# Kernel tuning notes

Hardware: AMD Instinct MI355X
Metric: run time of the kernel (lower is better)

## Reference

```python
import jax, jax.numpy as jnp
import numpy as np

H, CM, CS = 8, 16, 32  # num_heads, hidden_mv_channels, hidden_s_channels
_INNER_IDX = np.array([0, 2, 3, 4, 8, 9, 10, 14])  # PGA multivector components without e0


def _make_basis():
    # 9 Pin(3,0,1)-equivariant linear maps on 16-dim multivectors:
    # 5 grade projections + 4 left-multiplications by e0 (grade k -> grade k+1 e0-blades).
    # Component order: [1, e0, e1, e2, e3, e01, e02, e03, e12, e13, e23, e012, e013, e023, e123, e0123]
    b = np.zeros((9, 16, 16), dtype=np.float32)
    grades = [[0], [1, 2, 3, 4], [5, 6, 7, 8, 9, 10], [11, 12, 13, 14], [15]]
    for k, idxs in enumerate(grades):
        for i in idxs:
            b[k, i, i] = 1.0
    e0maps = {5: [(0, 1)], 6: [(2, 5), (3, 6), (4, 7)], 7: [(8, 11), (9, 12), (10, 13)], 8: [(14, 15)]}
    for k, pairs in e0maps.items():
        for i, o in pairs:
            b[k, o, i] = 1.0
    return jnp.asarray(b)


BASIS = _make_basis()  # (9, 16_out_comp, 16_in_comp)


def equi_linear(mv, s, w_mv, w_s2mv, b_mv, w_mv2s, w_s2s, b_s):
    # mv: (..., c_in, 16); s: (..., s_in)
    out_mv = jnp.einsum('yai,ocy,...ci->...oa', BASIS, w_mv, mv)
    out_mv = out_mv.at[..., 0].add(jnp.einsum('...i,oi->...o', s, w_s2mv) + b_mv)
    out_s = (jnp.einsum('...c,sc->...s', mv[..., 0], w_mv2s)
             + jnp.einsum('...i,si->...s', s, w_s2s) + b_s)
    return out_mv, out_s


def reference(multivectors_kv, multivectors_q, scalars_kv, scalars_q,
              q_w_mv, q_w_s2mv, q_b_mv, q_w_mv2s, q_w_s2s, q_b_s,
              k_w_mv, k_w_s2mv, k_b_mv, k_w_mv2s, k_w_s2s, k_b_s,
              v_w_mv, v_w_s2mv, v_b_mv, v_w_mv2s, v_w_s2s, v_b_s,
              o_w_mv, o_w_s2mv, o_b_mv, o_w_mv2s, o_w_s2s, o_b_s):
    B, Q = multivectors_q.shape[0], multivectors_q.shape[1]
    q_mv, q_s = equi_linear(multivectors_q, scalars_q, q_w_mv, q_w_s2mv, q_b_mv, q_w_mv2s, q_w_s2s, q_b_s)
    k_mv, k_s = equi_linear(multivectors_kv, scalars_kv, k_w_mv, k_w_s2mv, k_b_mv, k_w_mv2s, k_w_s2s, k_b_s)
    v_mv, v_s = equi_linear(multivectors_kv, scalars_kv, v_w_mv, v_w_s2mv, v_b_mv, v_w_mv2s, v_w_s2s, v_b_s)
    # split heads; einops pattern '(hidden_channels num_heads)' => channel-major, head-minor
    q_mv = q_mv.reshape(B, Q, CM, H, 16).transpose(0, 3, 1, 2, 4)  # (B,H,Q,CM,16)
    q_s = q_s.reshape(B, Q, CS, H).transpose(0, 3, 1, 2)            # (B,H,Q,CS)
    # multi-query: single k/v head broadcast over H
    scale = 1.0 / jnp.sqrt(jnp.asarray(8 * CM + CS, dtype=q_mv.dtype))
    scores = (jnp.einsum('bhqcx,bkcx->bhqk', q_mv[..., _INNER_IDX], k_mv[..., _INNER_IDX])
              + jnp.einsum('bhqs,bks->bhqk', q_s, k_s)) * scale
    attn = jax.nn.softmax(scores, axis=-1)
    h_mv = jnp.einsum('bhqk,bkcx->bhqcx', attn, v_mv)
    h_s = jnp.einsum('bhqk,bkc->bhqc', attn, v_s)
    # merge heads; pattern '(n_heads hidden_channels)' => head-major
    h_mv = h_mv.transpose(0, 2, 1, 3, 4).reshape(B, Q, H * CM, 16)
    h_s = h_s.transpose(0, 2, 1, 3).reshape(B, Q, H * CS)
    out_mv, out_s = equi_linear(h_mv, h_s, o_w_mv, o_w_s2mv, o_b_mv, o_w_mv2s, o_w_s2s, o_b_s)
    return out_mv, out_s


def setup_inputs():
    key = jax.random.key(0)
    ks = jax.random.split(key, 32)
    B, NQ, NKV, IN_MV, IN_S = 4, 2048, 2048, 16, 32
    w = 0.05  # weight scale to keep attention logits sane

    def rn(k, shape, s=1.0):
        return jax.random.normal(k, shape, dtype=jnp.float32) * s

    return {
        'multivectors_kv': rn(ks[0], (B, NKV, IN_MV, 16)),
        'multivectors_q': rn(ks[1], (B, NQ, IN_MV, 16)),
        'scalars_kv': rn(ks[2], (B, NKV, IN_S)),
        'scalars_q': rn(ks[3], (B, NQ, IN_S)),
        'q_w_mv': rn(ks[4], (CM * H, IN_MV, 9), w),
        'q_w_s2mv': rn(ks[5], (CM * H, IN_S), w),
        'q_b_mv': jnp.zeros((CM * H,), jnp.float32),
        'q_w_mv2s': rn(ks[6], (CS * H, IN_MV), w),
        'q_w_s2s': rn(ks[7], (CS * H, IN_S), w),
        'q_b_s': jnp.zeros((CS * H,), jnp.float32),
        'k_w_mv': rn(ks[8], (CM, IN_MV, 9), w),
        'k_w_s2mv': rn(ks[9], (CM, IN_S), w),
        'k_b_mv': jnp.zeros((CM,), jnp.float32),
        'k_w_mv2s': rn(ks[10], (CS, IN_MV), w),
        'k_w_s2s': rn(ks[11], (CS, IN_S), w),
        'k_b_s': jnp.zeros((CS,), jnp.float32),
        'v_w_mv': rn(ks[12], (CM, IN_MV, 9), w),
        'v_w_s2mv': rn(ks[13], (CM, IN_S), w),
        'v_b_mv': jnp.zeros((CM,), jnp.float32),
        'v_w_mv2s': rn(ks[14], (CS, IN_MV), w),
        'v_w_s2s': rn(ks[15], (CS, IN_S), w),
        'v_b_s': jnp.zeros((CS,), jnp.float32),
        'o_w_mv': rn(ks[16], (16, CM * H, 9), w),
        'o_w_s2mv': rn(ks[17], (16, CS * H), w),
        'o_b_mv': jnp.zeros((16,), jnp.float32),
        'o_w_mv2s': rn(ks[18], (32, CM * H), w),
        'o_w_s2s': rn(ks[19], (32, CS * H), w),
        'o_b_s': jnp.zeros((32,), jnp.float32),
    }
```

## Files before the change

kernel.cpp:

```cpp
#include <hip/hip_runtime.h>
#include <hip/hip_bf16.h>
#include <math.h>

#define NB   4
#define NQL  2048
#define NKVL 2048
#define HN   8
#define DQK  160
#define DV   288
#define QT   256
#define KTL  64
#define KLP  168

#define SCALE 0.07905694150420949f

typedef __attribute__((ext_vector_type(8)))  short short8;
typedef __attribute__((ext_vector_type(4)))  float f32x4;
typedef __attribute__((ext_vector_type(16))) float f32x16;

__constant__ int c_grade[16] = {0,1,1,1,1,2,2,2,2,2,2,3,3,3,3,4};
__constant__ int c_inner[8]  = {0,2,3,4,8,9,10,14};
__constant__ int c_esrc[16]  = {-1,0,-1,-1,-1,2,3,4,-1,-1,-1,8,9,10,-1,14};
__constant__ int c_ey[16]    = {0,5,0,0,0,6,6,6,0,0,0,7,7,7,0,8};

__device__ __forceinline__ ushort f2bf(float v) {
  __hip_bfloat16 h = __float2bfloat16(v);
  union { __hip_bfloat16 b; ushort u; } cv; cv.b = h; return cv.u;
}

__device__ __forceinline__ void gload16(const void* g, void* l) {
  __builtin_amdgcn_global_load_lds(
      (const __attribute__((address_space(1))) unsigned int*)g,
      (__attribute__((address_space(3))) unsigned int*)l, 16, 0, 0);
}

#define KWMV   0
#define KS2MV  2304
#define KMV2S  2816
#define KS2S   3328
#define KBMV   4352
#define KBS    4368
#define VWMV   4400
#define VS2MV  6704
#define VMV2S  7216
#define VS2S   7728
#define VBMV   8752
#define VBS    8768
#define WLSZ   8800
#define XSTR   289
#define OSTR   456
#define KVPOS  8

__device__ __forceinline__ void kv_accum(const float* wL, const float* xL,
                                         int f, float acc[KVPOS]) {
  if (f < 160) {
    if (f < 128) {
      int c = f >> 3, a = c_inner[f & 7], y = c_grade[a];
      float bias = (a == 0) ? wL[KBMV + c] : 0.f;
#pragma unroll
      for (int p = 0; p < KVPOS; p++) acc[p] = bias;
      for (int ci = 0; ci < 16; ci++) {
        float w = wL[KWMV + (c*16 + ci)*9 + y];
#pragma unroll
        for (int p = 0; p < KVPOS; p++) acc[p] += w * xL[p*XSTR + ci*16 + a];
      }
      if (a == 0) {
        for (int i2 = 0; i2 < 32; i2++) {
          float w = wL[KS2MV + c*32 + i2];
#pragma unroll
          for (int p = 0; p < KVPOS; p++) acc[p] += w * xL[p*XSTR + 256 + i2];
        }
      }
    } else {
      int si = f - 128;
      float bias = wL[KBS + si];
#pragma unroll
      for (int p = 0; p < KVPOS; p++) acc[p] = bias;
      for (int ci = 0; ci < 16; ci++) {
        float w = wL[KMV2S + si*16 + ci];
#pragma unroll
        for (int p = 0; p < KVPOS; p++) acc[p] += w * xL[p*XSTR + ci*16];
      }
      for (int i2 = 0; i2 < 32; i2++) {
        float w = wL[KS2S + si*32 + i2];
#pragma unroll
        for (int p = 0; p < KVPOS; p++) acc[p] += w * xL[p*XSTR + 256 + i2];
      }
    }
  } else {
    int g = f - 160;
    if (g < 256) {
      int c = g >> 4, a = g & 15, y = c_grade[a];
      float bias = (a == 0) ? wL[VBMV + c] : 0.f;
#pragma unroll
      for (int p = 0; p < KVPOS; p++) acc[p] = bias;
      for (int ci = 0; ci < 16; ci++) {
        float w = wL[VWMV + (c*16 + ci)*9 + y];
#pragma unroll
        for (int p = 0; p < KVPOS; p++) acc[p] += w * xL[p*XSTR + ci*16 + a];
      }
      int sa = c_esrc[a];
      if (sa >= 0) {
        int ey = c_ey[a];
        for (int ci = 0; ci < 16; ci++) {
          float w = wL[VWMV + (c*16 + ci)*9 + ey];
#pragma unroll
          for (int p = 0; p < KVPOS; p++) acc[p] += w * xL[p*XSTR + ci*16 + sa];
        }
      }
      if (a == 0) {
        for (int i2 = 0; i2 < 32; i2++) {
          float w = wL[VS2MV + c*32 + i2];
#pragma unroll
          for (int p = 0; p < KVPOS; p++) acc[p] += w * xL[p*XSTR + 256 + i2];
        }
      }
    } else {
      int si = g - 256;
      float bias = wL[VBS + si];
#pragma unroll
      for (int p = 0; p < KVPOS; p++) acc[p] = bias;
      for (int ci = 0; ci < 16; ci++) {
        float w = wL[VMV2S + si*16 + ci];
#pragma unroll
        for (int p = 0; p < KVPOS; p++) acc[p] += w * xL[p*XSTR + ci*16];
      }
      for (int i2 = 0; i2 < 32; i2++) {
        float w = wL[VS2S + si*32 + i2];
#pragma unroll
        for (int p = 0; p < KVPOS; p++) acc[p] += w * xL[p*XSTR + 256 + i2];
      }
    }
  }
}

__global__ __launch_bounds__(256) void proj_kv_kernel(
    const float* __restrict__ mv_kv, const float* __restrict__ s_kv,
    const float* __restrict__ kw_mv, const float* __restrict__ kw_s2mv, const float* __restrict__ kb_mv,
    const float* __restrict__ kw_mv2s, const float* __restrict__ kw_s2s, const float* __restrict__ kb_s,
    const float* __restrict__ vw_mv, const float* __restrict__ vw_s2mv, const float* __restrict__ vb_mv,
    const float* __restrict__ vw_mv2s, const float* __restrict__ vw_s2s, const float* __restrict__ vb_s,
    ushort* __restrict__ Kf, ushort* __restrict__ VfT)
{
  __shared__ float wL[WLSZ];
  __shared__ float xL[KVPOS*XSTR];
  int t = threadIdx.x;
  for (int i = t; i < 2304; i += 256) wL[KWMV + i] = kw_mv[i];
  for (int i = t; i < 512;  i += 256) wL[KS2MV + i] = kw_s2mv[i];
  for (int i = t; i < 512;  i += 256) wL[KMV2S + i] = kw_mv2s[i];
  for (int i = t; i < 1024; i += 256) wL[KS2S + i] = kw_s2s[i];
  if (t < 16) wL[KBMV + t] = kb_mv[t];
  if (t < 32) wL[KBS + t] = kb_s[t];
  for (int i = t; i < 2304; i += 256) wL[VWMV + i] = vw_mv[i];
  for (int i = t; i < 512;  i += 256) wL[VS2MV + i] = vw_s2mv[i];
  for (int i = t; i < 512;  i += 256) wL[VMV2S + i] = vw_mv2s[i];
  for (int i = t; i < 1024; i += 256) wL[VS2S + i] = vw_s2s[i];
  if (t < 16) wL[VBMV + t] = vb_mv[t];
  if (t < 32) wL[VBS + t] = vb_s[t];

  int p0 = blockIdx.x * KVPOS;
  for (int i = t; i < KVPOS*256; i += 256) {
    int p = i >> 8, c = i & 255;
    xL[p*XSTR + c] = mv_kv[(size_t)(p0 + p)*256 + c];
  }
  if (t < KVPOS*32) {
    int p = t >> 5, c = t & 31;
    xL[p*XSTR + 256 + c] = s_kv[(size_t)(p0 + p)*32 + c];
  }
  __syncthreads();

  float acc0[KVPOS], acc1[KVPOS];
  kv_accum(wL, xL, t, acc0);
  if (t < 192) kv_accum(wL, xL, 256 + t, acc1);
  __syncthreads();

  ushort* oL = (ushort*)xL;
#pragma unroll
  for (int p = 0; p < KVPOS; p++) oL[p*OSTR + t] = f2bf(acc0[p]);
  if (t < 192) {
#pragma unroll
    for (int p = 0; p < KVPOS; p++) oL[p*OSTR + 256 + t] = f2bf(acc1[p]);
  }
  __syncthreads();

  int b = p0 >> 11, kv0 = p0 & 2047;
  for (int it = 0; it < 3; it++) {
    int j = t + it*256;
    if (j < KVPOS*80) {
      int p = j / 80, fp = j - p*80;
      uint u = (uint)oL[p*OSTR + 2*fp] | ((uint)oL[p*OSTR + 2*fp + 1] << 16);
      *(uint*)(Kf + (size_t)(p0 + p)*DQK + 2*fp) = u;
    }
  }
  for (int it = 0; it < 5; it++) {
    int j = t + it*256;
    if (j < DV*(KVPOS/2)) {
      int g = j >> 2, pp = j & 3;
      uint u = (uint)oL[(2*pp)*OSTR + 160 + g] | ((uint)oL[(2*pp+1)*OSTR + 160 + g] << 16);
      int kv = kv0 + 2*pp;
      int pos = (kv & ~63) + ((((kv >> 3) & 7) ^ (g & 7)) << 3) + (kv & 7);
      *(uint*)(VfT + ((size_t)b*DV + g)*NKVL + pos) = u;
    }
  }
}

#define OWT_SZ 34816
#define QWT_MV 0
#define QWT_S  20480
#define QBT    61440
#define QWT_SZ 62720
__global__ __launch_bounds__(256) void prep_w_kernel(
    const float* __restrict__ ow_mv, const float* __restrict__ ow_s2mv,
    const float* __restrict__ ow_mv2s, const float* __restrict__ ow_s2s,
    float* __restrict__ owT,
    const float* __restrict__ qw_mv, const float* __restrict__ qw_s2mv, const float* __restrict__ qb_mv,
    const float* __restrict__ qw_mv2s, const float* __restrict__ qw_s2s, const float* __restrict__ qb_s,
    float* __restrict__ qwT)
{
  int i = blockIdx.x*256 + threadIdx.x;
  if (i < OWT_SZ) {
    if (i < 18432) {
      int y = i / 2048, r = i & 2047, ch = r >> 4, o = r & 15;
      owT[i] = ow_mv[(size_t)(o*128 + ch)*9 + y];
    } else if (i < 22528) {
      int r = i - 18432, jj = r >> 4, o = r & 15;
      owT[i] = ow_s2mv[o*256 + jj];
    } else if (i < 26624) {
      int r = i - 22528, ch = r >> 5, si = r & 31;
      owT[i] = ow_mv2s[si*128 + ch];
    } else {
      int r = i - 26624, jj = r >> 5, si = r & 31;
      owT[i] = ow_s2s[si*256 + jj];
    }
    return;
  }
  int j = i - OWT_SZ;
  if (j >= QWT_SZ) return;
  if (j < QWT_S) {
    int ci = j / 1280, r = j - ci*1280, h = r / 160, f0 = r - h*160;
    float v;
    if (f0 < 128) {
      int c = f0 >> 3, a = c_inner[f0 & 7], y = c_grade[a];
      v = qw_mv[((c*HN + h)*16 + ci)*9 + y];
    } else {
      v = qw_mv2s[((f0 - 128)*HN + h)*16 + ci];
    }
    qwT[j] = v;
  } else if (j < QBT) {
    int k = j - QWT_S;
    int i2 = k / 1280, r = k - i2*1280, h = r / 160, f0 = r - h*160;
    float v;
    if (f0 < 128) {
      int c = f0 >> 3, a = c_inner[f0 & 7];
      v = (a == 0) ? qw_s2mv[(c*HN + h)*32 + i2] : 0.f;
    } else {
      v = qw_s2s[((f0 - 128)*HN + h)*32 + i2];
    }
    qwT[j] = v;
  } else {
    int r = j - QBT, h = r / 160, f0 = r - h*160;
    float v;
    if (f0 < 128) {
      int c = f0 >> 3, a = c_inner[f0 & 7];
      v = (a == 0) ? qb_mv[c*HN + h] : 0.f;
    } else {
      v = qb_s[(f0 - 128)*HN + h];
    }
    qwT[j] = v;
  }
}

#define QPOS 8
__global__ __launch_bounds__(320) void proj_q_kernel(
    const float* __restrict__ mv_q, const float* __restrict__ s_q,
    const float* __restrict__ qwT,
    ushort* __restrict__ Qf)
{
  __shared__ float xL[QPOS*XSTR];
  int t = threadIdx.x;
  int p0 = blockIdx.x * QPOS;
  for (int i = t; i < QPOS*256; i += 320) {
    int p = i >> 8, c = i & 255;
    xL[p*XSTR + c] = mv_q[(size_t)(p0 + p)*256 + c];
  }
  if (t < QPOS*32) {
    int p = t >> 5, c = t & 31;
    xL[p*XSTR + 256 + c] = s_q[(size_t)(p0 + p)*32 + c];
  }
  __syncthreads();

  int f0 = t % 160;
  int h0 = t / 160;
  int a = (f0 < 128) ? c_inner[f0 & 7] : 0;

  float acc[4][QPOS];
#pragma unroll
  for (int k = 0; k < 4; k++) {
    float bv = qwT[QBT + (h0 + 2*k)*160 + f0];
#pragma unroll
    for (int p = 0; p < QPOS; p++) acc[k][p] = bv;
  }
  for (int ci = 0; ci < 16; ci++) {
    float w0 = qwT[QWT_MV + (ci*HN + h0    )*160 + f0];
    float w1 = qwT[QWT_MV + (ci*HN + h0 + 2)*160 + f0];
    float w2 = qwT[QWT_MV + (ci*HN + h0 + 4)*160 + f0];
    float w3 = qwT[QWT_MV + (ci*HN + h0 + 6)*160 + f0];
#pragma unroll
    for (int p = 0; p < QPOS; p++) {
      float xv = xL[p*XSTR + ci*16 + a];
      acc[0][p] += w0*xv; acc[1][p] += w1*xv;
      acc[2][p] += w2*xv; acc[3][p] += w3*xv;
    }
  }
  for (int i2 = 0; i2 < 32; i2++) {
    float w0 = qwT[QWT_S + (i2*HN + h0    )*160 + f0];
    float w1 = qwT[QWT_S + (i2*HN + h0 + 2)*160 + f0];
    float w2 = qwT[QWT_S + (i2*HN + h0 + 4)*160 + f0];
    float w3 = qwT[QWT_S + (i2*HN + h0 + 6)*160 + f0];
#pragma unroll
    for (int p = 0; p < QPOS; p++) {
      float xv = xL[p*XSTR + 256 + i2];
      acc[0][p] += w0*xv; acc[1][p] += w1*xv;
      acc[2][p] += w2*xv; acc[3][p] += w3*xv;
    }
  }

  int b = p0 >> 11, q0 = p0 & 2047;
#pragma unroll
  for (int k = 0; k < 4; k++) {
    int h = h0 + 2*k;
    ushort* qdst = Qf + ((size_t)(b*HN + h)*NQL + q0)*DQK + f0;
#pragma unroll
    for (int p = 0; p < QPOS; p++)
      qdst[p*DQK] = f2bf(acc[k][p] * SCALE);
  }
}

__global__ __launch_bounds__(512, 1) void attn_kernel(
    const ushort* __restrict__ Kf,
    const ushort* __restrict__ VfT,
    const ushort* __restrict__ Qf,
    float* __restrict__ Hf)
{
  __shared__ ushort kL[2][KTL*KLP];
  __shared__ ushort vtL[2][DV*KTL];

  const int NT = NQL/QT;
  int bid = blockIdx.x;
  int swz = (bid & 7) * 32 + (bid >> 3);
  int bh = swz / NT;
  int qt = swz - bh*NT;
  int b = bh >> 3, h = bh & 7;
  int t = threadIdx.x, w = t >> 6, l = t & 63;
  int ql = l & 31, hb = l >> 5;

  const ushort* kb = Kf  + (size_t)b*NKVL*DQK;
  const ushort* vb = VfT + (size_t)b*DV*NKVL;

  const ushort* qrow = Qf + ((size_t)bh*NQL + (size_t)qt*QT + w*32 + ql)*DQK + hb*8;
  short8 qf[10];
#pragma unroll
  for (int ks = 0; ks < 10; ks++)
    qf[ks] = *(const short8*)(qrow + ks*16);

  f32x16 oA[9];
#pragma unroll
  for (int i = 0; i < 9; i++) oA[i] = (f32x16)(0.f);
  float m = -INFINITY, lsum = 0.f;

#define STAGE(KT, BUF) do {                                            \
    const ushort* kg_ = kb + (size_t)(KT)*KTL*DQK;                     \
    char* kd_ = (char*)&kL[BUF][0];                                    \
    for (int c_ = w; c_ < 21; c_ += 8) {                               \
      int off_ = c_*1024 + l*16;                                       \
      int row_ = off_ / 336;                                           \
      int bc_  = off_ - row_*336;                                      \
      const ushort* ga_ = kg_ + row_*DQK + ((bc_ < 320) ? (bc_ >> 1) : 0); \
      gload16(ga_, kd_ + c_*1024);                                     \
    }                                                                  \
    const ushort* vg_ = vb + (size_t)(KT)*KTL;                         \
    char* vd_ = (char*)&vtL[BUF][0];                                   \
    for (int c_ = w; c_ < 36; c_ += 8) {                               \
      int off_ = c_*1024 + l*16;                                       \
      int d_  = off_ >> 7;                                             \
      int bc_ = off_ & 127;                                            \
      const ushort* ga_ = vg_ + (size_t)d_*NKVL + (bc_ >> 1);          \
      gload16(ga_, vd_ + c_*1024);                                     \
    }                                                                  \
  } while (0)

  STAGE(0, 0);
  __syncthreads();

  for (int kt = 0; kt < NKVL/KTL; kt++) {
    int cur = kt & 1;
    if (kt + 1 < NKVL/KTL) STAGE(kt + 1, cur ^ 1);

    const ushort* kbuf  = &kL[cur][0];
    const ushort* vtbuf = &vtL[cur][0];

    f32x16 sA[2];
    __builtin_amdgcn_s_setprio(1);
#pragma unroll
    for (int kvb = 0; kvb < 2; kvb++) {
      sA[kvb] = (f32x16)(0.f);
      const ushort* krow = kbuf + (ql + 32*kvb)*KLP + hb*8;
#pragma unroll
      for (int ks = 0; ks < 10; ks++) {
        short8 kf = *(const short8*)(krow + ks*16);
        sA[kvb] = __builtin_amdgcn_mfma_f32_32x32x16_bf16(kf, qf[ks], sA[kvb], 0, 0, 0);
      }
    }
    __builtin_amdgcn_s_setprio(0);

    float tm = sA[0][0];
#pragma unroll
    for (int kvb = 0; kvb < 2; kvb++)
#pragma unroll
      for (int r = 0; r < 16; r++) tm = fmaxf(tm, sA[kvb][r]);
    tm = fmaxf(tm, __shfl_xor(tm, 32));
    if (!__all(tm - m <= 8.0f)) {
      float nm = fmaxf(m, tm);
      float ef = __expf(m - nm);
      lsum *= ef;
#pragma unroll
      for (int i = 0; i < 9; i++)
#pragma unroll
        for (int r = 0; r < 16; r++) oA[i][r] *= ef;
      m = nm;
    }
    float rs = 0.f;
#pragma unroll
    for (int kvb = 0; kvb < 2; kvb++)
#pragma unroll
      for (int r = 0; r < 16; r++) {
        float p = __expf(sA[kvb][r] - m);
        sA[kvb][r] = p;
        rs += p;
      }
    rs += __shfl_xor(rs, 32);
    lsum += rs;

    unsigned int pk[2][8];
#pragma unroll
    for (int kvb = 0; kvb < 2; kvb++)
#pragma unroll
      for (int k = 0; k < 8; k++) {
        unsigned int r_;
        asm("v_cvt_pk_bf16_f32 %0, %1, %2" : "=v"(r_) : "v"(sA[kvb][2*k]), "v"(sA[kvb][2*k+1]));
        pk[kvb][k] = r_;
      }

#pragma unroll
    for (int s = 0; s < 4; s++) {
      const int n0 = 2*s, n1 = 2*s + 1;
      unsigned int u[4];
#pragma unroll
      for (int p = 0; p < 4; p++) {
        unsigned int Xa = pk[n0 >> 2][(p & 1) + 2*(n0 & 3)];
        unsigned int Xb = pk[n1 >> 2][(p & 1) + 2*(n1 & 3)];
        int src = ql + 32*(p >> 1);
        unsigned int ua = __shfl((int)Xa, src);
        unsigned int ub = __shfl((int)Xb, src);
        u[p] = hb ? ub : ua;
      }
      union { unsigned int uu[4]; short8 s8; } pf;
      pf.uu[0] = u[0]; pf.uu[1] = u[1]; pf.uu[2] = u[2]; pf.uu[3] = u[3];
      __builtin_amdgcn_s_setprio(1);
#pragma unroll
      for (int db = 0; db < 9; db++) {
        int d = ql + 32*db;
        int col = (((2*s + hb) ^ (d & 7)) << 3);
        short8 vf = *(const short8*)(vtbuf + d*KTL + col);
        oA[db] = __builtin_amdgcn_mfma_f32_32x32x16_bf16(vf, pf.s8, oA[db], 0, 0, 0);
      }
      __builtin_amdgcn_s_setprio(0);
    }
    __syncthreads();
  }
#undef STAGE

  float inv = 1.0f / lsum;
  int q = qt*QT + w*32 + ql;
  float* orow = Hf + (((size_t)b*NQL + q)*HN + h)*DV;
#pragma unroll
  for (int db = 0; db < 9; db++)
#pragma unroll
    for (int j = 0; j < 4; j++) {
      int d0 = 32*db + 8*j + 4*hb;
      float4 st = make_float4(oA[db][4*j]*inv, oA[db][4*j+1]*inv,
                              oA[db][4*j+2]*inv, oA[db][4*j+3]*inv);
      *(float4*)(orow + d0) = st;
    }
}

#define HSTR2 2308
#define OPOS2 8
__global__ __launch_bounds__(512) void proj_o_kernel(
    const float* __restrict__ Hf,
    const float* __restrict__ owT,
    const float* __restrict__ ob_mv, const float* __restrict__ ob_s,
    float* __restrict__ outp)
{
  __shared__ float hL[OPOS2*HSTR2];
  __shared__ float pL[256*8];
  __shared__ float sP[8*48*8];
  int t = threadIdx.x;
  int p0 = blockIdx.x * OPOS2;
  for (int i = t; i < OPOS2*2304/4; i += 512) {
    int idx = i*4; int p = idx / 2304; int c = idx - p*2304;
    *(float4*)(hL + p*HSTR2 + c) = *(const float4*)(Hf + (size_t)(p0 + p)*2304 + c);
  }
  __syncthreads();

  const float* mvT   = owT;
  const float* s2mvT = owT + 18432;
  const float* mv2sT = owT + 22528;
  const float* s2sT  = owT + 26624;

  int o = t & 15, a = (t >> 4) & 15, seg = t >> 8;
  int oa = o*16 + a;
  int y = c_grade[a], sa = c_esrc[a], ey = c_ey[a];
  float acc[OPOS2];
#pragma unroll
  for (int p = 0; p < OPOS2; p++) acc[p] = 0.f;
  for (int ch = seg*64; ch < seg*64 + 64; ch++) {
    int xb = (ch >> 4)*288 + (ch & 15)*16;
    float w1 = mvT[y*2048 + ch*16 + o];
#pragma unroll
    for (int p = 0; p < OPOS2; p++) acc[p] += w1 * hL[p*HSTR2 + xb + a];
    if (sa >= 0) {
      float w2 = mvT[ey*2048 + ch*16 + o];
#pragma unroll
      for (int p = 0; p < OPOS2; p++) acc[p] += w2 * hL[p*HSTR2 + xb + sa];
    }
  }
  if (seg == 1) {
#pragma unroll
    for (int p = 0; p < OPOS2; p++) pL[oa*8 + p] = acc[p];
  }
  __syncthreads();
  if (seg == 0) {
#pragma unroll
    for (int p = 0; p < OPOS2; p++) acc[p] += pL[oa*8 + p];
  }

  int v = t >> 6, u = t & 63;
  float sacc[OPOS2];
#pragma unroll
  for (int p = 0; p < OPOS2; p++) sacc[p] = 0.f;
  if (u < 32) {
    int si = u;
    for (int ch = v*16; ch < v*16 + 16; ch++) {
      float w = mv2sT[ch*32 + si];
      int xb = (ch >> 4)*288 + (ch & 15)*16;
#pragma unroll
      for (int p = 0; p < OPOS2; p++) sacc[p] += w * hL[p*HSTR2 + xb];
    }
    for (int jj = v*32; jj < v*32 + 32; jj++) {
      float w = s2sT[jj*32 + si];
      int xb = (jj >> 5)*288 + 256 + (jj & 31);
#pragma unroll
      for (int p = 0; p < OPOS2; p++) sacc[p] += w * hL[p*HSTR2 + xb];
    }
  } else if (u < 48) {
    int o2 = u - 32;
    for (int jj = v*32; jj < v*32 + 32; jj++) {
      float w = s2mvT[jj*16 + o2];
      int xb = (jj >> 5)*288 + 256 + (jj & 31);
#pragma unroll
      for (int p = 0; p < OPOS2; p++) sacc[p] += w * hL[p*HSTR2 + xb];
    }
  }
  if (u < 48) {
#pragma unroll
    for (int p = 0; p < OPOS2; p++) sP[(v*48 + u)*8 + p] = sacc[p];
  }
  __syncthreads();

  if (seg == 0) {
    if (a == 0) {
      float bv = ob_mv[o];
#pragma unroll
      for (int p = 0; p < OPOS2; p++) {
        float s = bv;
#pragma unroll
        for (int vv = 0; vv < 8; vv++) s += sP[(vv*48 + 32 + o)*8 + p];
        acc[p] += s;
      }
    }
#pragma unroll
    for (int p = 0; p < OPOS2; p++) pL[oa*8 + p] = acc[p];
  }
  __syncthreads();
  for (int i = t; i < 256*OPOS2; i += 512) {
    int p = i >> 8, c = i & 255;
    outp[(size_t)(p0 + p)*256 + c] = pL[c*8 + p];
  }
  if (t >= 256 && t < 256 + 32) {
    int si = t - 256;
    float bv = ob_s[si];
    float* out_s = outp + (size_t)NB*NQL*256;
#pragma unroll
    for (int p = 0; p < OPOS2; p++) {
      float s = bv;
#pragma unroll
      for (int vv = 0; vv < 8; vv++) s += sP[(vv*48 + si)*8 + p];
      out_s[(size_t)(p0 + p)*32 + si] = s;
    }
  }
}

extern "C" void kernel_launch(void* const* d_in, const int* in_sizes, int n_in,
                              void* d_out, int out_size, void* d_ws, size_t ws_size,
                              hipStream_t stream)
{
  const float* mv_kv = (const float*)d_in[0];
  const float* mv_q  = (const float*)d_in[1];
  const float* s_kv  = (const float*)d_in[2];
  const float* s_q   = (const float*)d_in[3];

  ushort* Kf  = (ushort*)d_ws;
  ushort* VfT = Kf  + (size_t)NB*NKVL*DQK;
  ushort* Qf  = VfT + (size_t)NB*DV*NKVL;
  float*  Hf  = (float*)(Qf + (size_t)NB*HN*NQL*DQK);
  float*  owT = Hf + (size_t)NB*NQL*HN*DV;
  float*  qwT = owT + OWT_SZ;

  prep_w_kernel<<<(OWT_SZ + QWT_SZ + 255)/256, 256, 0, stream>>>(
      (const float*)d_in[22], (const float*)d_in[23],
      (const float*)d_in[25], (const float*)d_in[26], owT,
      (const float*)d_in[4], (const float*)d_in[5], (const float*)d_in[6],
      (const float*)d_in[7], (const float*)d_in[8], (const float*)d_in[9],
      qwT);
  proj_kv_kernel<<<NB*NKVL/KVPOS, 256, 0, stream>>>(mv_kv, s_kv,
      (const float*)d_in[10], (const float*)d_in[11], (const float*)d_in[12],
      (const float*)d_in[13], (const float*)d_in[14], (const float*)d_in[15],
      (const float*)d_in[16], (const float*)d_in[17], (const float*)d_in[18],
      (const float*)d_in[19], (const float*)d_in[20], (const float*)d_in[21],
      Kf, VfT);
  proj_q_kernel<<<NB*NQL/QPOS, 320, 0, stream>>>(mv_q, s_q, qwT, Qf);
  attn_kernel<<<NB*HN*(NQL/QT), 512, 0, stream>>>(Kf, VfT, Qf, Hf);
  proj_o_kernel<<<NB*NQL/OPOS2, 512, 0, stream>>>(Hf, owT,
      (const float*)d_in[24], (const float*)d_in[27],
      (float*)d_out);
}
```

Before: 335.8 us.

## Halve attention query and KV tiles to run two blocks per CU

Changes the attention kernel from 512-thread blocks over 256 queries and 64-key tiles to 256-thread blocks over 128 queries and 32-key tiles, with launch bounds allowing two blocks per CU. The staging loops, the V transpose swizzle in the KV projection and the PV column XOR are rewritten for the smaller tile, and the block swizzle is widened for the doubled grid. The aim is more resident waves and smaller LDS per block, so loads and softmax can overlap better across blocks. In exchange each tile does half the MFMA work per barrier, so there are twice as many synchronisations and rescale checks per query, plus more Q-fragment and K/V reload traffic across blocks.

```diff
diff --git a/kernel.cpp b/kernel.cpp
--- a/kernel.cpp
+++ b/kernel.cpp
@@ -8,8 +8,8 @@
 #define HN   8
 #define DQK  160
 #define DV   288
-#define QT   256
-#define KTL  64
+#define QT   128
+#define KTL  32
 #define KLP  168
 
 #define SCALE 0.07905694150420949f
@@ -198,7 +198,7 @@
       int g = j >> 2, pp = j & 3;
       uint u = (uint)oL[(2*pp)*OSTR + 160 + g] | ((uint)oL[(2*pp+1)*OSTR + 160 + g] << 16);
       int kv = kv0 + 2*pp;
-      int pos = (kv & ~63) + ((((kv >> 3) & 7) ^ (g & 7)) << 3) + (kv & 7);
+      int pos = (kv & ~31) + ((((kv >> 3) & 3) ^ (g & 3)) << 3) + (kv & 7);
       *(uint*)(VfT + ((size_t)b*DV + g)*NKVL + pos) = u;
     }
   }
@@ -336,7 +336,7 @@
   }
 }
 
-__global__ __launch_bounds__(512, 1) void attn_kernel(
+__global__ __launch_bounds__(256, 2) void attn_kernel(
     const ushort* __restrict__ Kf,
     const ushort* __restrict__ VfT,
     const ushort* __restrict__ Qf,
@@ -347,7 +347,7 @@
 
   const int NT = NQL/QT;
   int bid = blockIdx.x;
-  int swz = (bid & 7) * 32 + (bid >> 3);
+  int swz = (bid & 7) * 64 + (bid >> 3);
   int bh = swz / NT;
   int qt = swz - bh*NT;
   int b = bh >> 3, h = bh & 7;
@@ -371,21 +371,27 @@
 #define STAGE(KT, BUF) do {                                            \
     const ushort* kg_ = kb + (size_t)(KT)*KTL*DQK;                     \
     char* kd_ = (char*)&kL[BUF][0];                                    \
-    for (int c_ = w; c_ < 21; c_ += 8) {                               \
-      int off_ = c_*1024 + l*16;                                       \
-      int row_ = off_ / 336;                                           \
-      int bc_  = off_ - row_*336;                                      \
-      const ushort* ga_ = kg_ + row_*DQK + ((bc_ < 320) ? (bc_ >> 1) : 0); \
-      gload16(ga_, kd_ + c_*1024);                                     \
+    for (int it_ = 0; it_ < 3; it_++) {                                \
+      int ch_ = t + it_*256;                                           \
+      if (ch_ < 672) {                                                 \
+        int off_ = ch_*16;                                             \
+        int row_ = off_ / 336;                                         \
+        int bc_  = off_ - row_*336;                                    \
+        const ushort* ga_ = kg_ + row_*DQK + ((bc_ < 320) ? (bc_ >> 1) : 0); \
+        gload16(ga_, kd_ + off_);                                      \
+      }                                                                \
     }                                                                  \
     const ushort* vg_ = vb + (size_t)(KT)*KTL;                         \
     char* vd_ = (char*)&vtL[BUF][0];                                   \
-    for (int c_ = w; c_ < 36; c_ += 8) {                               \
-      int off_ = c_*1024 + l*16;                                       \
-      int d_  = off_ >> 7;                                             \
-      int bc_ = off_ & 127;                                            \
-      const ushort* ga_ = vg_ + (size_t)d_*NKVL + (bc_ >> 1);          \
-      gload16(ga_, vd_ + c_*1024);                                     \
+    for (int it_ = 0; it_ < 5; it_++) {                                \
+      int ch_ = t + it_*256;                                           \
+      if (ch_ < 1152) {                                                \
+        int off_ = ch_*16;                                             \
+        int d_  = off_ >> 6;                                           \
+        int bc_ = off_ & 63;                                           \
+        const ushort* ga_ = vg_ + (size_t)d_*NKVL + (bc_ >> 1);        \
+        gload16(ga_, vd_ + off_);                                      \
+      }                                                                \
     }                                                                  \
   } while (0)
 
@@ -399,25 +405,22 @@
     const ushort* kbuf  = &kL[cur][0];
     const ushort* vtbuf = &vtL[cur][0];
 
-    f32x16 sA[2];
+    f32x16 sA;
+    sA = (f32x16)(0.f);
     __builtin_amdgcn_s_setprio(1);
-#pragma unroll
-    for (int kvb = 0; kvb < 2; kvb++) {
-      sA[kvb] = (f32x16)(0.f);
-      const ushort* krow = kbuf + (ql + 32*kvb)*KLP + hb*8;
+    {
+      const ushort* krow = kbuf + ql*KLP + hb*8;
 #pragma unroll
       for (int ks = 0; ks < 10; ks++) {
         short8 kf = *(const short8*)(krow + ks*16);
-        sA[kvb] = __builtin_amdgcn_mfma_f32_32x32x16_bf16(kf, qf[ks], sA[kvb], 0, 0, 0);
+        sA = __builtin_amdgcn_mfma_f32_32x32x16_bf16(kf, qf[ks], sA, 0, 0, 0);
       }
     }
     __builtin_amdgcn_s_setprio(0);
 
-    float tm = sA[0][0];
-#pragma unroll
-    for (int kvb = 0; kvb < 2; kvb++)
-#pragma unroll
-      for (int r = 0; r < 16; r++) tm = fmaxf(tm, sA[kvb][r]);
+    float tm = sA[0];
+#pragma unroll
+    for (int r = 1; r < 16; r++) tm = fmaxf(tm, sA[r]);
     tm = fmaxf(tm, __shfl_xor(tm, 32));
     if (!__all(tm - m <= 8.0f)) {
       float nm = fmaxf(m, tm);
@@ -431,34 +434,30 @@
     }
     float rs = 0.f;
 #pragma unroll
-    for (int kvb = 0; kvb < 2; kvb++)
-#pragma unroll
-      for (int r = 0; r < 16; r++) {
-        float p = __expf(sA[kvb][r] - m);
-        sA[kvb][r] = p;
-        rs += p;
-      }
+    for (int r = 0; r < 16; r++) {
+      float p = __expf(sA[r] - m);
+      sA[r] = p;
+      rs += p;
+    }
     rs += __shfl_xor(rs, 32);
     lsum += rs;
 
-    unsigned int pk[2][8];
-#pragma unroll
-    for (int kvb = 0; kvb < 2; kvb++)
-#pragma unroll
-      for (int k = 0; k < 8; k++) {
-        unsigned int r_;
-        asm("v_cvt_pk_bf16_f32 %0, %1, %2" : "=v"(r_) : "v"(sA[kvb][2*k]), "v"(sA[kvb][2*k+1]));
-        pk[kvb][k] = r_;
-      }
-
-#pragma unroll
-    for (int s = 0; s < 4; s++) {
+    unsigned int pk8[8];
+#pragma unroll
+    for (int k = 0; k < 8; k++) {
+      unsigned int r_;
+      asm("v_cvt_pk_bf16_f32 %0, %1, %2" : "=v"(r_) : "v"(sA[2*k]), "v"(sA[2*k+1]));
+      pk8[k] = r_;
+    }
+
+#pragma unroll
+    for (int s = 0; s < 2; s++) {
       const int n0 = 2*s, n1 = 2*s + 1;
       unsigned int u[4];
 #pragma unroll
       for (int p = 0; p < 4; p++) {
-        unsigned int Xa = pk[n0 >> 2][(p & 1) + 2*(n0 & 3)];
-        unsigned int Xb = pk[n1 >> 2][(p & 1) + 2*(n1 & 3)];
+        unsigned int Xa = pk8[(p & 1) + 2*n0];
+        unsigned int Xb = pk8[(p & 1) + 2*n1];
         int src = ql + 32*(p >> 1);
         unsigned int ua = __shfl((int)Xa, src);
         unsigned int ub = __shfl((int)Xb, src);
@@ -470,7 +469,7 @@
 #pragma unroll
       for (int db = 0; db < 9; db++) {
         int d = ql + 32*db;
-        int col = (((2*s + hb) ^ (d & 7)) << 3);
+        int col = (((2*s + hb) ^ (d & 3)) << 3);
         short8 vf = *(const short8*)(vtbuf + d*KTL + col);
         oA[db] = __builtin_amdgcn_mfma_f32_32x32x16_bf16(vf, pf.s8, oA[db], 0, 0, 0);
       }
@@ -640,7 +639,7 @@
       (const float*)d_in[19], (const float*)d_in[20], (const float*)d_in[21],
       Kf, VfT);
   proj_q_kernel<<<NB*NQL/QPOS, 320, 0, stream>>>(mv_q, s_q, qwT, Qf);
-  attn_kernel<<<NB*HN*(NQL/QT), 512, 0, stream>>>(Kf, VfT, Qf, Hf);
+  attn_kernel<<<NB*HN*(NQL/QT), 256, 0, stream>>>(Kf, VfT, Qf, Hf);
   proj_o_kernel<<<NB*NQL/OPOS2, 512, 0, stream>>>(Hf, owT,
       (const float*)d_in[24], (const float*)d_in[27],
       (float*)d_out);
```

New measurement: 351.4 us. 4.7% more time.
